# Kernel optimization log

Measured on AMD Instinct MI355X. Metric: run time of the kernel, lower is better.

## Reference

```python
import jax, jax.numpy as jnp
import numpy as np

EMBED_DIM = 512
NUM_HEADS = 32


def setup_inputs() -> dict:
    key = jax.random.key(0)
    k0, k1, k2, k3, k4 = jax.random.split(key, 5)
    bsz, n = 4, 512
    x = jax.random.normal(k0, (n, bsz, EMBED_DIM), dtype=jnp.float32)
    pos = jax.random.normal(k1, (bsz, n, 3), dtype=jnp.float32) * 3.0
    padding_mask = jnp.ones((bsz, n), dtype=bool)  # True = valid node
    s = 0.02
    Wq = jax.random.normal(k2, (EMBED_DIM, EMBED_DIM), dtype=jnp.float32) * s
    Wk = jax.random.normal(k3, (EMBED_DIM, EMBED_DIM), dtype=jnp.float32) * s
    Wv = jax.random.normal(k4, (EMBED_DIM, EMBED_DIM), dtype=jnp.float32) * s
    return {"x": x, "pos": pos, "padding_mask": padding_mask, "Wq": Wq, "Wk": Wk, "Wv": Wv}


def reference(x, pos, padding_mask, Wq, Wk, Wv):
    n, bsz, E = x.shape
    H = NUM_HEADS
    d = E // H
    scaling = d ** (-0.5)

    xb = jnp.transpose(x, (1, 0, 2))  # (bsz, n, E)

    # pairwise unit-direction vectors: delta[b,i,j] = pos[b,j] - pos[b,i]
    delta = pos[:, None, :, :] - pos[:, :, None, :]  # (b, n, n, 3)
    dist = jnp.sqrt(jnp.sum(delta * delta, axis=-1) + 1e-12)  # safe norm (diag ~0)
    delta = delta / (dist[..., None] + 1e-5)

    def heads(W):  # torch Linear: y = x @ W^T
        return (xb @ W.T).reshape(bsz, n, H, d).transpose(0, 2, 1, 3)  # (b, h, n, d)

    q = heads(Wq) * scaling
    k = heads(Wk)
    v = heads(Wv)

    attn = jnp.einsum("bhid,bhjd->bhij", q, k)  # (b, h, n, n)
    min_val = jnp.finfo(attn.dtype).min
    attn = jnp.where(padding_mask[:, None, :, None], attn, min_val)
    probs = jax.nn.softmax(attn, axis=-1)  # (b, h, n, n)

    delta = jnp.where(padding_mask[:, :, None, None], delta, 0.0)

    # out[b,i,c,h,d] = sum_j probs[b,h,i,j] * delta[b,i,j,c] * v[b,h,j,d]
    out = jnp.einsum("bhij,bijc,bhjd->bichd", probs, delta, v)
    return out.reshape(bsz, n, 3, E)
```

## Files before the change

### kernel.cpp

```cpp
#include <hip/hip_runtime.h>
#include <math.h>

#define EMBED 512
#define NHEAD 32
#define HDIM  16
#define BSZ   4
#define SEQ   512
#define QKV_ELEMS (BSZ*NHEAD*SEQ*HDIM)
#define PLANE (BSZ*SEQ*SEQ)

typedef __fp16 h2 __attribute__((ext_vector_type(2)));
typedef __fp16 h4 __attribute__((ext_vector_type(4)));
typedef __fp16 h8 __attribute__((ext_vector_type(8)));
typedef float f32x4 __attribute__((ext_vector_type(4)));
union H4 { h4 v; h2 p[2]; };
union H8 { h8 v; h4 q[2]; h2 p[4]; };

#define XROW 72

__global__ __launch_bounds__(256) void projdelta_kernel(
    const float* __restrict__ x,  const float* __restrict__ Wq,
    const float* __restrict__ Wk, const float* __restrict__ Wv,
    const float* __restrict__ pos,
    __fp16* __restrict__ qkv, __fp16* __restrict__ Uxy, __fp16* __restrict__ Uz)
{
  __shared__ __fp16 lds[16384];
  const int bx = blockIdx.x;
  const int tid = threadIdx.x;

  if (bx >= 128) {
    const int pb  = bx - 128;
    const int swz = (pb & 7) * 96 + (pb >> 3);
    const int m0  = (swz / 24) * 64;
    const int r24 = swz % 24;
    const int n0  = (r24 & 7) * 64;
    const int z   = r24 >> 3;
    __fp16* Xs = lds;
    __fp16* Ws = lds + 64*XROW;
    const float* Wz = (z==0) ? Wq : (z==1) ? Wk : Wv;
    const float scw = (z==0) ? 0.25f * 1.44269504089f : 1.0f;

    const int l = tid & 63, w = tid >> 6;
    const int il = l & 15, g = l >> 4;

    f32x4 acc[4];
    #pragma unroll
    for (int u=0;u<4;++u) acc[u] = (f32x4){0.f,0.f,0.f,0.f};

    const int srow = tid >> 2, sq = tid & 3;
    const float* xrow = x  + (size_t)(m0+srow)*512;
    const float* wrow = Wz + (size_t)(n0+srow)*512;

    float4 xA[2], xB[2], wA[2], wB[2];
#define LOADG(K0) { \
      _Pragma("unroll") \
      for (int j=0;j<2;++j) { \
        const int s = sq*4 + 2*j; \
        xA[j] = *(const float4*)&xrow[(K0) + s*4]; \
        xB[j] = *(const float4*)&xrow[(K0) + s*4 + 4]; \
        wA[j] = *(const float4*)&wrow[(K0) + s*4]; \
        wB[j] = *(const float4*)&wrow[(K0) + s*4 + 4]; } }

    LOADG(0);
    for (int k0 = 0; k0 < 512; k0 += 64) {
      __syncthreads();
      #pragma unroll
      for (int j=0;j<2;++j) {
        const int s  = sq*4 + 2*j;
        H8 ox;
        ox.p[0] = __builtin_amdgcn_cvt_pkrtz(xA[j].x, xA[j].y);
        ox.p[1] = __builtin_amdgcn_cvt_pkrtz(xA[j].z, xA[j].w);
        ox.p[2] = __builtin_amdgcn_cvt_pkrtz(xB[j].x, xB[j].y);
        ox.p[3] = __builtin_amdgcn_cvt_pkrtz(xB[j].z, xB[j].w);
        *(h8*)&Xs[srow*XROW + s*4] = ox.v;
        H8 ow;
        ow.p[0] = __builtin_amdgcn_cvt_pkrtz(wA[j].x*scw, wA[j].y*scw);
        ow.p[1] = __builtin_amdgcn_cvt_pkrtz(wA[j].z*scw, wA[j].w*scw);
        ow.p[2] = __builtin_amdgcn_cvt_pkrtz(wB[j].x*scw, wB[j].y*scw);
        ow.p[3] = __builtin_amdgcn_cvt_pkrtz(wB[j].z*scw, wB[j].w*scw);
        *(h8*)&Ws[srow*XROW + s*4] = ow.v;
      }
      __syncthreads();
      if (k0 + 64 < 512) LOADG(k0 + 64);
      #pragma unroll
      for (int kh=0;kh<4;++kh) {
        const int sl = kh*4 + g;
        h4 a, bb[4];
        a = *(const h4*)&Xs[(w*16+il)*XROW + sl*4];
        #pragma unroll
        for (int u=0;u<4;++u)
          bb[u] = *(const h4*)&Ws[(u*16+il)*XROW + sl*4];
        #pragma unroll
        for (int u=0;u<4;++u)
          acc[u] = __builtin_amdgcn_mfma_f32_16x16x16f16(a, bb[u], acc[u], 0,0,0);
      }
    }
#undef LOADG

    __syncthreads();
    #pragma unroll
    for (int u=0;u<4;++u) {
      const int row0 = w*16 + 4*g;
      #pragma unroll
      for (int r=0;r<4;++r)
        lds[(row0+r)*72 + u*16 + il] = (__fp16)acc[u][r];
    }
    __syncthreads();
    {
      const int ml = tid >> 2, hs = tid & 3;
      const h8 c0 = *(const h8*)&lds[ml*72 + hs*16];
      const h8 c1 = *(const h8*)&lds[ml*72 + hs*16 + 8];
      const int m = m0 + ml;
      const int b = m & 3, i = m >> 2;
      const int h = (n0 >> 4) + hs;
      __fp16* dst = qkv + (size_t)z*QKV_ELEMS + ((size_t)(b*NHEAD+h)*SEQ + i)*HDIM;
      *(h8*)dst = c0;
      *(h8*)(dst+8) = c1;
    }
    return;
  }

  float* pxs = (float*)lds;
  float* pys = pxs + SEQ;
  float* pzs = pys + SEQ;
  const int db = bx;
  const int b = db >> 5, it = db & 31;
  const float* posg = pos + (size_t)b*SEQ*3;
  {
    float pv[6];
    #pragma unroll
    for (int u=0;u<6;++u) pv[u] = posg[tid*6+u];
    pxs[2*tid]=pv[0];   pys[2*tid]=pv[1];   pzs[2*tid]=pv[2];
    pxs[2*tid+1]=pv[3]; pys[2*tid+1]=pv[4]; pzs[2*tid+1]=pv[5];
  }
  __syncthreads();
  const int lane = tid & 63, w = tid >> 6;
  const int il = lane & 15, sl = lane >> 4;
  const int i = it*16 + il;
  const float pix = pxs[i], piy = pys[i], piz = pzs[i];
  const size_t xybase = (size_t)(b*32 + it)*16384 + il*8;
  const size_t zbase  = (size_t)(b*32 + it)*8192  + il*4;
  #pragma unroll
  for (int u=0;u<8;++u) {
    const int s = u*16 + w*4 + sl;
    const int j = s*4;
    const f32x4 jx = *(const f32x4*)&pxs[j];
    const f32x4 jy = *(const f32x4*)&pys[j];
    const f32x4 jz = *(const f32x4*)&pzs[j];
    float wx[4], wy[4], wz[4];
    #pragma unroll
    for (int e=0;e<4;++e) {
      const float dx = jx[e]-pix, dy = jy[e]-piy, dz = jz[e]-piz;
      const float d2 = fmaf(dx,dx, fmaf(dy,dy, dz*dz)) + 1e-12f;
      const float dist = __builtin_amdgcn_sqrtf(d2);
      const float inv = __builtin_amdgcn_rcpf(dist + 1e-5f);
      wx[e]=inv*dx; wy[e]=inv*dy; wz[e]=inv*dz;
    }
    H8 oxy;
    oxy.p[0]=__builtin_amdgcn_cvt_pkrtz(wx[0],wx[1]); oxy.p[1]=__builtin_amdgcn_cvt_pkrtz(wx[2],wx[3]);
    oxy.p[2]=__builtin_amdgcn_cvt_pkrtz(wy[0],wy[1]); oxy.p[3]=__builtin_amdgcn_cvt_pkrtz(wy[2],wy[3]);
    H4 oz;
    oz.p[0]=__builtin_amdgcn_cvt_pkrtz(wz[0],wz[1]); oz.p[1]=__builtin_amdgcn_cvt_pkrtz(wz[2],wz[3]);
    *(h8*)&Uxy[xybase + (size_t)s*128] = oxy.v;
    *(h4*)&Uz[zbase + (size_t)s*64]    = oz.v;
  }
}

#define KROW 40
#define VT1 (16*520)

__global__ __launch_bounds__(256) void attn_kernel(
    const __fp16* __restrict__ q, const __fp16* __restrict__ k,
    const __fp16* __restrict__ v, const __fp16* __restrict__ Uxy,
    const __fp16* __restrict__ Uz, float* __restrict__ out)
{
  __shared__ __fp16 Ks2[SEQ*KROW];
  __shared__ __fp16 Vt[2*VT1];

  const int tid = threadIdx.x;
  const int h0 = blockIdx.y*2, b = blockIdx.z;
  const size_t hb0 = (size_t)(b*NHEAD + h0    )*SEQ*HDIM;
  const size_t hb1 = (size_t)(b*NHEAD + h0 + 1)*SEQ*HDIM;

  {
    const int r0 = tid*2;
    H8 k0a,k0b,k0c,k0d, k1a,k1b,k1c,k1d;
    const h8* kg0 = (const h8*)(k + hb0 + (size_t)r0*HDIM);
    const h8* kg1 = (const h8*)(k + hb1 + (size_t)r0*HDIM);
    k0a.v=kg0[0]; k0b.v=kg0[1]; k0c.v=kg0[2]; k0d.v=kg0[3];
    k1a.v=kg1[0]; k1b.v=kg1[1]; k1c.v=kg1[2]; k1d.v=kg1[3];
    H8 t;
    t.q[0]=k0a.q[0]; t.q[1]=k1a.q[0]; *(h8*)&Ks2[r0*KROW + 0]  = t.v;
    t.q[0]=k0a.q[1]; t.q[1]=k1a.q[1]; *(h8*)&Ks2[r0*KROW + 8]  = t.v;
    t.q[0]=k0b.q[0]; t.q[1]=k1b.q[0]; *(h8*)&Ks2[r0*KROW + 16] = t.v;
    t.q[0]=k0b.q[1]; t.q[1]=k1b.q[1]; *(h8*)&Ks2[r0*KROW + 24] = t.v;
    t.q[0]=k0c.q[0]; t.q[1]=k1c.q[0]; *(h8*)&Ks2[(r0+1)*KROW + 0]  = t.v;
    t.q[0]=k0c.q[1]; t.q[1]=k1c.q[1]; *(h8*)&Ks2[(r0+1)*KROW + 8]  = t.v;
    t.q[0]=k0d.q[0]; t.q[1]=k1d.q[0]; *(h8*)&Ks2[(r0+1)*KROW + 16] = t.v;
    t.q[0]=k0d.q[1]; t.q[1]=k1d.q[1]; *(h8*)&Ks2[(r0+1)*KROW + 24] = t.v;

    #pragma unroll
    for (int hh=0; hh<2; ++hh) {
      const h8* vg = (const h8*)(v + (hh ? hb1 : hb0) + (size_t)r0*HDIM);
      const h8 va = vg[0], vb = vg[1], vc = vg[2], vd = vg[3];
      #pragma unroll
      for (int dd=0;dd<8;++dd) {
        h2 t0; t0[0]=va[dd]; t0[1]=vc[dd];
        *(h2*)&Vt[hh*VT1 + dd*520 + r0] = t0;
        h2 t1; t1[0]=vb[dd]; t1[1]=vd[dd];
        *(h2*)&Vt[hh*VT1 + (dd+8)*520 + r0] = t1;
      }
    }
  }

  const int l = tid & 63, w = tid >> 6;
  const int il = l & 15, g = l >> 4;
  const int i = blockIdx.x*64 + w*16 + il;

  const h4 qf0 = *(const h4*)(q + hb0 + (size_t)i*HDIM + g*4);
  const h4 qf1 = *(const h4*)(q + hb1 + (size_t)i*HDIM + g*4);
  const __fp16* uxyp = Uxy + (size_t)(b*32 + (i>>4))*16384 + il*8;
  const __fp16* uzp  = Uz  + (size_t)(b*32 + (i>>4))*8192  + il*4;

  float zl0 = 0.f, zl1 = 0.f;
  const f32x4 zero4 = {0.f,0.f,0.f,0.f};
  f32x4 a00 = zero4, a01 = zero4, a02 = zero4;
  f32x4 a10 = zero4, a11 = zero4, a12 = zero4;

  struct Buf { H8 uxy; H4 uz; H8 kf; h4 vf0, vf1; };
  struct ST  { f32x4 s0, s1; };
  Buf A, B, C, D;
  ST stA, stB, stC, stD;

#define LOADT(J, B_) { \
    const int s_ = (J)*4 + g; \
    B_.uxy.v = *(const h8*)&uxyp[(size_t)s_*128]; \
    B_.uz.v  = *(const h4*)&uzp[(size_t)s_*64]; \
    B_.kf.v  = *(const h8*)&Ks2[((J)*16+il)*KROW + g*8]; \
    B_.vf0 = *(const h4*)&Vt[il*520 + s_*4]; \
    B_.vf1 = *(const h4*)&Vt[VT1 + il*520 + s_*4]; }

#define QKT(B_, S_) { \
    S_.s0 = __builtin_amdgcn_mfma_f32_16x16x16f16(B_.kf.q[0], qf0, zero4, 0,0,0); \
    S_.s1 = __builtin_amdgcn_mfma_f32_16x16x16f16(B_.kf.q[1], qf1, zero4, 0,0,0); }

#define SMPV(S_, B_) { \
    const float p00 = __builtin_amdgcn_exp2f(S_.s0[0]), p01 = __builtin_amdgcn_exp2f(S_.s0[1]); \
    const float p02 = __builtin_amdgcn_exp2f(S_.s0[2]), p03 = __builtin_amdgcn_exp2f(S_.s0[3]); \
    const float p10 = __builtin_amdgcn_exp2f(S_.s1[0]), p11 = __builtin_amdgcn_exp2f(S_.s1[1]); \
    const float p12 = __builtin_amdgcn_exp2f(S_.s1[2]), p13 = __builtin_amdgcn_exp2f(S_.s1[3]); \
    zl0 += (p00+p01) + (p02+p03); \
    zl1 += (p10+p11) + (p12+p13); \
    H4 ph0, ph1; \
    ph0.p[0] = __builtin_amdgcn_cvt_pkrtz(p00,p01); ph0.p[1] = __builtin_amdgcn_cvt_pkrtz(p02,p03); \
    ph1.p[0] = __builtin_amdgcn_cvt_pkrtz(p10,p11); ph1.p[1] = __builtin_amdgcn_cvt_pkrtz(p12,p13); \
    H4 f0, f1, f2; \
    f0.p[0] = ph0.p[0]*B_.uxy.p[0]; f0.p[1] = ph0.p[1]*B_.uxy.p[1]; \
    f1.p[0] = ph0.p[0]*B_.uxy.p[2]; f1.p[1] = ph0.p[1]*B_.uxy.p[3]; \
    f2.p[0] = ph0.p[0]*B_.uz.p[0];  f2.p[1] = ph0.p[1]*B_.uz.p[1]; \
    a00 = __builtin_amdgcn_mfma_f32_16x16x16f16(B_.vf0, f0.v, a00, 0,0,0); \
    a01 = __builtin_amdgcn_mfma_f32_16x16x16f16(B_.vf0, f1.v, a01, 0,0,0); \
    a02 = __builtin_amdgcn_mfma_f32_16x16x16f16(B_.vf0, f2.v, a02, 0,0,0); \
    H4 g0, g1, g2; \
    g0.p[0] = ph1.p[0]*B_.uxy.p[0]; g0.p[1] = ph1.p[1]*B_.uxy.p[1]; \
    g1.p[0] = ph1.p[0]*B_.uxy.p[2]; g1.p[1] = ph1.p[1]*B_.uxy.p[3]; \
    g2.p[0] = ph1.p[0]*B_.uz.p[0];  g2.p[1] = ph1.p[1]*B_.uz.p[1]; \
    a10 = __builtin_amdgcn_mfma_f32_16x16x16f16(B_.vf1, g0.v, a10, 0,0,0); \
    a11 = __builtin_amdgcn_mfma_f32_16x16x16f16(B_.vf1, g1.v, a11, 0,0,0); \
    a12 = __builtin_amdgcn_mfma_f32_16x16x16f16(B_.vf1, g2.v, a12, 0,0,0); }

  __syncthreads();
  LOADT(0, A);
  LOADT(1, B);
  LOADT(2, C);
  QKT(A, stA);

  for (int jt = 0; jt < 32; jt += 4) {
    const int j3 = (jt+3) & 31, j4 = (jt+4) & 31;
    const int j5 = (jt+5) & 31, j6 = (jt+6) & 31;
    LOADT(j3, D);  QKT(B, stB);  SMPV(stA, A);
    LOADT(j4, A);  QKT(C, stC);  SMPV(stB, B);
    LOADT(j5, B);  QKT(D, stD);  SMPV(stC, C);
    LOADT(j6, C);  QKT(A, stA);  SMPV(stD, D);
  }
#undef LOADT
#undef QKT
#undef SMPV

  {
    float zz = zl0;
    zz += __shfl_xor(zz, 16, 64);
    zz += __shfl_xor(zz, 32, 64);
    const float invZ = __builtin_amdgcn_rcpf(zz);
    f32x4 r0 = a00*invZ, r1 = a01*invZ, r2 = a02*invZ;
    float* ob = out + ((size_t)(b*SEQ + i)*3)*EMBED + h0*HDIM + 4*g;
    *(f32x4*)(ob)           = r0;
    *(f32x4*)(ob + EMBED)   = r1;
    *(f32x4*)(ob + 2*EMBED) = r2;
  }
  {
    float zz = zl1;
    zz += __shfl_xor(zz, 16, 64);
    zz += __shfl_xor(zz, 32, 64);
    const float invZ = __builtin_amdgcn_rcpf(zz);
    f32x4 r0 = a10*invZ, r1 = a11*invZ, r2 = a12*invZ;
    float* ob = out + ((size_t)(b*SEQ + i)*3)*EMBED + (h0+1)*HDIM + 4*g;
    *(f32x4*)(ob)           = r0;
    *(f32x4*)(ob + EMBED)   = r1;
    *(f32x4*)(ob + 2*EMBED) = r2;
  }
}

extern "C" void kernel_launch(void* const* d_in, const int* in_sizes, int n_in,
                              void* d_out, int out_size, void* d_ws, size_t ws_size,
                              hipStream_t stream) {
  const float* x   = (const float*)d_in[0];
  const float* pos = (const float*)d_in[1];
  const float* Wq  = (const float*)d_in[3];
  const float* Wk  = (const float*)d_in[4];
  const float* Wv  = (const float*)d_in[5];
  float* out = (float*)d_out;

  __fp16* qkv = (__fp16*)d_ws;
  __fp16* Uxy = qkv + 3*(size_t)QKV_ELEMS;
  __fp16* Uz  = Uxy + 2*(size_t)PLANE;

  projdelta_kernel<<<896, 256, 0, stream>>>(x, Wq, Wk, Wv, pos, qkv, Uxy, Uz);
  attn_kernel<<<dim3(SEQ/64, NHEAD/2, BSZ), 256, 0, stream>>>(
      qkv, qkv + QKV_ELEMS, qkv + 2*(size_t)QKV_ELEMS, Uxy, Uz, out);
}
```

Measured before the change: 39.96 us.

## Process one head per attention block instead of two heads

The attention kernel now handles a single head per block, which halves shared memory for K and V and doubles the grid along the head axis. Before, each block amortized the per-pair direction loads (Uxy/Uz) across two heads. Now every head re-reads those direction planes from global memory, roughly doubling that traffic. In exchange, blocks use fewer registers and less LDS, which should raise occupancy and parallelism.

```diff
diff --git a/kernel.cpp b/kernel.cpp
--- a/kernel.cpp
+++ b/kernel.cpp
@@ -166,50 +166,34 @@
   }
 }
 
-#define KROW 40
-#define VT1 (16*520)
-
 __global__ __launch_bounds__(256) void attn_kernel(
     const __fp16* __restrict__ q, const __fp16* __restrict__ k,
     const __fp16* __restrict__ v, const __fp16* __restrict__ Uxy,
     const __fp16* __restrict__ Uz, float* __restrict__ out)
 {
-  __shared__ __fp16 Ks2[SEQ*KROW];
-  __shared__ __fp16 Vt[2*VT1];
+  __shared__ __fp16 Ks[SEQ*20];
+  __shared__ __fp16 Vt[16*520];
 
   const int tid = threadIdx.x;
-  const int h0 = blockIdx.y*2, b = blockIdx.z;
-  const size_t hb0 = (size_t)(b*NHEAD + h0    )*SEQ*HDIM;
-  const size_t hb1 = (size_t)(b*NHEAD + h0 + 1)*SEQ*HDIM;
+  const int h = blockIdx.y, b = blockIdx.z;
+  const size_t hb = (size_t)(b*NHEAD + h)*SEQ*HDIM;
 
   {
     const int r0 = tid*2;
-    H8 k0a,k0b,k0c,k0d, k1a,k1b,k1c,k1d;
-    const h8* kg0 = (const h8*)(k + hb0 + (size_t)r0*HDIM);
-    const h8* kg1 = (const h8*)(k + hb1 + (size_t)r0*HDIM);
-    k0a.v=kg0[0]; k0b.v=kg0[1]; k0c.v=kg0[2]; k0d.v=kg0[3];
-    k1a.v=kg1[0]; k1b.v=kg1[1]; k1c.v=kg1[2]; k1d.v=kg1[3];
-    H8 t;
-    t.q[0]=k0a.q[0]; t.q[1]=k1a.q[0]; *(h8*)&Ks2[r0*KROW + 0]  = t.v;
-    t.q[0]=k0a.q[1]; t.q[1]=k1a.q[1]; *(h8*)&Ks2[r0*KROW + 8]  = t.v;
-    t.q[0]=k0b.q[0]; t.q[1]=k1b.q[0]; *(h8*)&Ks2[r0*KROW + 16] = t.v;
-    t.q[0]=k0b.q[1]; t.q[1]=k1b.q[1]; *(h8*)&Ks2[r0*KROW + 24] = t.v;
-    t.q[0]=k0c.q[0]; t.q[1]=k1c.q[0]; *(h8*)&Ks2[(r0+1)*KROW + 0]  = t.v;
-    t.q[0]=k0c.q[1]; t.q[1]=k1c.q[1]; *(h8*)&Ks2[(r0+1)*KROW + 8]  = t.v;
-    t.q[0]=k0d.q[0]; t.q[1]=k1d.q[0]; *(h8*)&Ks2[(r0+1)*KROW + 16] = t.v;
-    t.q[0]=k0d.q[1]; t.q[1]=k1d.q[1]; *(h8*)&Ks2[(r0+1)*KROW + 24] = t.v;
-
-    #pragma unroll
-    for (int hh=0; hh<2; ++hh) {
-      const h8* vg = (const h8*)(v + (hh ? hb1 : hb0) + (size_t)r0*HDIM);
-      const h8 va = vg[0], vb = vg[1], vc = vg[2], vd = vg[3];
-      #pragma unroll
-      for (int dd=0;dd<8;++dd) {
-        h2 t0; t0[0]=va[dd]; t0[1]=vc[dd];
-        *(h2*)&Vt[hh*VT1 + dd*520 + r0] = t0;
-        h2 t1; t1[0]=vb[dd]; t1[1]=vd[dd];
-        *(h2*)&Vt[hh*VT1 + (dd+8)*520 + r0] = t1;
-      }
+    const h8* kg = (const h8*)(k + hb + (size_t)r0*HDIM);
+    const h8 ka = kg[0], kb = kg[1], kc = kg[2], kd = kg[3];
+    *(h8*)&Ks[r0*20]        = ka;
+    *(h8*)&Ks[r0*20+8]      = kb;
+    *(h8*)&Ks[(r0+1)*20]    = kc;
+    *(h8*)&Ks[(r0+1)*20+8]  = kd;
+    const h8* vg = (const h8*)(v + hb + (size_t)r0*HDIM);
+    const h8 va = vg[0], vb = vg[1], vc = vg[2], vd = vg[3];
+    #pragma unroll
+    for (int dd=0;dd<8;++dd) {
+      h2 t0; t0[0]=va[dd]; t0[1]=vc[dd];
+      *(h2*)&Vt[dd*520 + r0] = t0;
+      h2 t1; t1[0]=vb[dd]; t1[1]=vd[dd];
+      *(h2*)&Vt[(dd+8)*520 + r0] = t1;
     }
   }
 
@@ -217,57 +201,42 @@
   const int il = l & 15, g = l >> 4;
   const int i = blockIdx.x*64 + w*16 + il;
 
-  const h4 qf0 = *(const h4*)(q + hb0 + (size_t)i*HDIM + g*4);
-  const h4 qf1 = *(const h4*)(q + hb1 + (size_t)i*HDIM + g*4);
+  const h4 qf = *(const h4*)(q + hb + (size_t)i*HDIM + g*4);
   const __fp16* uxyp = Uxy + (size_t)(b*32 + (i>>4))*16384 + il*8;
   const __fp16* uzp  = Uz  + (size_t)(b*32 + (i>>4))*8192  + il*4;
 
-  float zl0 = 0.f, zl1 = 0.f;
+  float zl = 0.f;
   const f32x4 zero4 = {0.f,0.f,0.f,0.f};
-  f32x4 a00 = zero4, a01 = zero4, a02 = zero4;
-  f32x4 a10 = zero4, a11 = zero4, a12 = zero4;
-
-  struct Buf { H8 uxy; H4 uz; H8 kf; h4 vf0, vf1; };
-  struct ST  { f32x4 s0, s1; };
+  f32x4 a0 = zero4, a1 = zero4, a2 = zero4;
+
+  struct Buf { H8 uxy; H4 uz; h4 kf, vf; };
   Buf A, B, C, D;
-  ST stA, stB, stC, stD;
+  f32x4 stA, stB, stC, stD;
 
 #define LOADT(J, B_) { \
     const int s_ = (J)*4 + g; \
     B_.uxy.v = *(const h8*)&uxyp[(size_t)s_*128]; \
     B_.uz.v  = *(const h4*)&uzp[(size_t)s_*64]; \
-    B_.kf.v  = *(const h8*)&Ks2[((J)*16+il)*KROW + g*8]; \
-    B_.vf0 = *(const h4*)&Vt[il*520 + s_*4]; \
-    B_.vf1 = *(const h4*)&Vt[VT1 + il*520 + s_*4]; }
+    B_.kf = *(const h4*)&Ks[((J)*16+il)*20 + g*4]; \
+    B_.vf = *(const h4*)&Vt[il*520 + s_*4]; }
 
 #define QKT(B_, S_) { \
-    S_.s0 = __builtin_amdgcn_mfma_f32_16x16x16f16(B_.kf.q[0], qf0, zero4, 0,0,0); \
-    S_.s1 = __builtin_amdgcn_mfma_f32_16x16x16f16(B_.kf.q[1], qf1, zero4, 0,0,0); }
+    S_ = __builtin_amdgcn_mfma_f32_16x16x16f16(B_.kf, qf, zero4, 0,0,0); }
 
 #define SMPV(S_, B_) { \
-    const float p00 = __builtin_amdgcn_exp2f(S_.s0[0]), p01 = __builtin_amdgcn_exp2f(S_.s0[1]); \
-    const float p02 = __builtin_amdgcn_exp2f(S_.s0[2]), p03 = __builtin_amdgcn_exp2f(S_.s0[3]); \
-    const float p10 = __builtin_amdgcn_exp2f(S_.s1[0]), p11 = __builtin_amdgcn_exp2f(S_.s1[1]); \
-    const float p12 = __builtin_amdgcn_exp2f(S_.s1[2]), p13 = __builtin_amdgcn_exp2f(S_.s1[3]); \
-    zl0 += (p00+p01) + (p02+p03); \
-    zl1 += (p10+p11) + (p12+p13); \
-    H4 ph0, ph1; \
-    ph0.p[0] = __builtin_amdgcn_cvt_pkrtz(p00,p01); ph0.p[1] = __builtin_amdgcn_cvt_pkrtz(p02,p03); \
-    ph1.p[0] = __builtin_amdgcn_cvt_pkrtz(p10,p11); ph1.p[1] = __builtin_amdgcn_cvt_pkrtz(p12,p13); \
+    const float p0 = __builtin_amdgcn_exp2f(S_[0]), p1 = __builtin_amdgcn_exp2f(S_[1]); \
+    const float p2 = __builtin_amdgcn_exp2f(S_[2]), p3 = __builtin_amdgcn_exp2f(S_[3]); \
+    zl += (p0+p1) + (p2+p3); \
+    H4 ph; \
+    ph.p[0] = __builtin_amdgcn_cvt_pkrtz(p0,p1); \
+    ph.p[1] = __builtin_amdgcn_cvt_pkrtz(p2,p3); \
     H4 f0, f1, f2; \
-    f0.p[0] = ph0.p[0]*B_.uxy.p[0]; f0.p[1] = ph0.p[1]*B_.uxy.p[1]; \
-    f1.p[0] = ph0.p[0]*B_.uxy.p[2]; f1.p[1] = ph0.p[1]*B_.uxy.p[3]; \
-    f2.p[0] = ph0.p[0]*B_.uz.p[0];  f2.p[1] = ph0.p[1]*B_.uz.p[1]; \
-    a00 = __builtin_amdgcn_mfma_f32_16x16x16f16(B_.vf0, f0.v, a00, 0,0,0); \
-    a01 = __builtin_amdgcn_mfma_f32_16x16x16f16(B_.vf0, f1.v, a01, 0,0,0); \
-    a02 = __builtin_amdgcn_mfma_f32_16x16x16f16(B_.vf0, f2.v, a02, 0,0,0); \
-    H4 g0, g1, g2; \
-    g0.p[0] = ph1.p[0]*B_.uxy.p[0]; g0.p[1] = ph1.p[1]*B_.uxy.p[1]; \
-    g1.p[0] = ph1.p[0]*B_.uxy.p[2]; g1.p[1] = ph1.p[1]*B_.uxy.p[3]; \
-    g2.p[0] = ph1.p[0]*B_.uz.p[0];  g2.p[1] = ph1.p[1]*B_.uz.p[1]; \
-    a10 = __builtin_amdgcn_mfma_f32_16x16x16f16(B_.vf1, g0.v, a10, 0,0,0); \
-    a11 = __builtin_amdgcn_mfma_f32_16x16x16f16(B_.vf1, g1.v, a11, 0,0,0); \
-    a12 = __builtin_amdgcn_mfma_f32_16x16x16f16(B_.vf1, g2.v, a12, 0,0,0); }
+    f0.p[0] = ph.p[0]*B_.uxy.p[0]; f0.p[1] = ph.p[1]*B_.uxy.p[1]; \
+    f1.p[0] = ph.p[0]*B_.uxy.p[2]; f1.p[1] = ph.p[1]*B_.uxy.p[3]; \
+    f2.p[0] = ph.p[0]*B_.uz.p[0];  f2.p[1] = ph.p[1]*B_.uz.p[1]; \
+    a0 = __builtin_amdgcn_mfma_f32_16x16x16f16(B_.vf, f0.v, a0, 0,0,0); \
+    a1 = __builtin_amdgcn_mfma_f32_16x16x16f16(B_.vf, f1.v, a1, 0,0,0); \
+    a2 = __builtin_amdgcn_mfma_f32_16x16x16f16(B_.vf, f2.v, a2, 0,0,0); }
 
   __syncthreads();
   LOADT(0, A);
@@ -287,28 +256,15 @@
 #undef QKT
 #undef SMPV
 
-  {
-    float zz = zl0;
-    zz += __shfl_xor(zz, 16, 64);
-    zz += __shfl_xor(zz, 32, 64);
-    const float invZ = __builtin_amdgcn_rcpf(zz);
-    f32x4 r0 = a00*invZ, r1 = a01*invZ, r2 = a02*invZ;
-    float* ob = out + ((size_t)(b*SEQ + i)*3)*EMBED + h0*HDIM + 4*g;
-    *(f32x4*)(ob)           = r0;
-    *(f32x4*)(ob + EMBED)   = r1;
-    *(f32x4*)(ob + 2*EMBED) = r2;
-  }
-  {
-    float zz = zl1;
-    zz += __shfl_xor(zz, 16, 64);
-    zz += __shfl_xor(zz, 32, 64);
-    const float invZ = __builtin_amdgcn_rcpf(zz);
-    f32x4 r0 = a10*invZ, r1 = a11*invZ, r2 = a12*invZ;
-    float* ob = out + ((size_t)(b*SEQ + i)*3)*EMBED + (h0+1)*HDIM + 4*g;
-    *(f32x4*)(ob)           = r0;
-    *(f32x4*)(ob + EMBED)   = r1;
-    *(f32x4*)(ob + 2*EMBED) = r2;
-  }
+  float zz = zl;
+  zz += __shfl_xor(zz, 16, 64);
+  zz += __shfl_xor(zz, 32, 64);
+  const float invZ = __builtin_amdgcn_rcpf(zz);
+  const f32x4 r0 = a0*invZ, r1 = a1*invZ, r2 = a2*invZ;
+  float* ob = out + ((size_t)(b*SEQ + i)*3)*EMBED + h*HDIM + 4*g;
+  *(f32x4*)(ob)           = r0;
+  *(f32x4*)(ob + EMBED)   = r1;
+  *(f32x4*)(ob + 2*EMBED) = r2;
 }
 
 extern "C" void kernel_launch(void* const* d_in, const int* in_sizes, int n_in,
@@ -326,6 +282,6 @@
   __fp16* Uz  = Uxy + 2*(size_t)PLANE;
 
   projdelta_kernel<<<896, 256, 0, stream>>>(x, Wq, Wk, Wv, pos, qkv, Uxy, Uz);
-  attn_kernel<<<dim3(SEQ/64, NHEAD/2, BSZ), 256, 0, stream>>>(
+  attn_kernel<<<dim3(SEQ/64, NHEAD, BSZ), 256, 0, stream>>>(
       qkv, qkv + QKV_ELEMS, qkv + 2*(size_t)QKV_ELEMS, Uxy, Uz, out);
 }
```

Result: slower. 41.33 us (+3.4%).
